# Optimization experiments

Measured on AMD Instinct MI355X. Metric: run time of the kernel, lower is better.

## Reference

```python
import jax, jax.numpy as jnp
import numpy as np

N, IN_DIM, OUT_DIM = 100000, 256, 256
EPS = 1e-6

def setup_inputs() -> dict:
    key = jax.random.key(0)
    ks = jax.random.split(key, 7)
    s = 1.0 / np.sqrt(IN_DIM)
    x = jax.random.normal(ks[0], (N, IN_DIM), dtype=jnp.float32)
    Wq = jax.random.uniform(ks[1], (IN_DIM, OUT_DIM), jnp.float32, -s, s)
    bq = jax.random.uniform(ks[2], (OUT_DIM,), jnp.float32, -s, s)
    Wk = jax.random.uniform(ks[3], (IN_DIM, OUT_DIM), jnp.float32, -s, s)
    bk = jax.random.uniform(ks[4], (OUT_DIM,), jnp.float32, -s, s)
    Wv = jax.random.uniform(ks[5], (IN_DIM, OUT_DIM), jnp.float32, -s, s)
    bv = jax.random.uniform(ks[6], (OUT_DIM,), jnp.float32, -s, s)
    return {"x": x, "Wq": Wq, "bq": bq, "Wk": Wk, "bk": bk, "Wv": Wv, "bv": bv}

def reference(x, Wq, bq, Wk, bk, Wv, bv):
    Q = jax.nn.relu(x @ Wq + bq)          # [N, d]
    K = jax.nn.relu(x @ Wk + bk)          # [N, d]
    V = x @ Wv + bv                       # [N, d]
    KV = jnp.einsum('nd,ne->de', K, V)    # [d, d]
    out = Q @ KV                          # [N, d]
    normalizer = Q @ K.sum(axis=0)[:, None].reshape(-1) [..., None] if False else (Q @ K.sum(axis=0)[:, None]) + EPS  # [N, 1]
    return out / normalizer
```

## Files before the change

### kernel.cpp

```cpp
#include <hip/hip_runtime.h>

typedef unsigned short u16;
typedef float f32x4 __attribute__((ext_vector_type(4)));
typedef short s16x8 __attribute__((ext_vector_type(8)));
typedef unsigned short u16x4 __attribute__((ext_vector_type(4)));

#define EPS 1e-6f

static __device__ __forceinline__ u16 f2bf(float f) {
  unsigned u = __float_as_uint(f);
  u += 0x7fffu + ((u >> 16) & 1u);
  return (u16)(u >> 16);
}
static __device__ __forceinline__ float bf2f(u16 h) {
  return __uint_as_float(((unsigned)h) << 16);
}

__global__ void wtrans_kernel(const float* __restrict__ Wq, const float* __restrict__ Wk,
                              const float* __restrict__ Wv,
                              u16* __restrict__ WqT, u16* __restrict__ WkT, u16* __restrict__ WvT) {
  int b = blockIdx.x;
  int mat = b >> 4, cg = b & 15;
  const float* W = mat == 0 ? Wq : (mat == 1 ? Wk : Wv);
  u16* WT = mat == 0 ? WqT : (mat == 1 ? WkT : WvT);
  int t = threadIdx.x;
  int c = cg * 16 + (t & 15);
  int k0 = (t >> 4) * 16;
  for (int i = 0; i < 16; ++i) {
    int k = k0 + i;
    WT[c * 256 + k] = f2bf(W[k * 256 + c]);
  }
}

__global__ __launch_bounds__(256, 2)
void qkv_kernel(const float* __restrict__ x,
                const u16* __restrict__ WqT, const u16* __restrict__ WkT, const u16* __restrict__ WvT,
                const float* __restrict__ bq, const float* __restrict__ bk, const float* __restrict__ bv,
                u16* __restrict__ Qb, u16* __restrict__ Kt, u16* __restrict__ Vt,
                int N, int NPAD) {
  __shared__ u16 xs[128][264];
  __shared__ u16 wst[128][40];
  const int tid = threadIdx.x;
  const int n0 = blockIdx.x * 128;

  for (int i = 0; i < 32; ++i) {
    int l = tid + i * 256;
    int row = l >> 6;
    int c4 = (l & 63) << 2;
    int n = n0 + row;
    float4 v = make_float4(0.f, 0.f, 0.f, 0.f);
    if (n < N) v = *(const float4*)(x + (size_t)n * 256 + c4);
    xs[row][c4 + 0] = f2bf(v.x);
    xs[row][c4 + 1] = f2bf(v.y);
    xs[row][c4 + 2] = f2bf(v.z);
    xs[row][c4 + 3] = f2bf(v.w);
  }

  const int wave = tid >> 6, lane = tid & 63;
  const int quad = lane >> 4, l16 = lane & 15;
  const int wr = (wave >> 1) * 64;
  const int wc = (wave & 1) * 64;

  for (int ph = 0; ph < 6; ++ph) {
    const int mat = ph >> 1;
    const int colBase = (ph & 1) * 128;
    const u16* WT = mat == 0 ? WqT : (mat == 1 ? WkT : WvT);
    const float* bias = mat == 0 ? bq : (mat == 1 ? bk : bv);
    f32x4 acc[4][4] = {};
    for (int kc = 0; kc < 256; kc += 32) {
      __syncthreads();
      for (int i = 0; i < 2; ++i) {
        int l = tid + i * 256;
        int col = l >> 2;
        int seg = (l & 3) << 3;
        *(s16x8*)&wst[col][seg] = *(const s16x8*)&WT[(size_t)(colBase + col) * 256 + kc + seg];
      }
      __syncthreads();
      s16x8 a[4], b[4];
      for (int f = 0; f < 4; ++f) a[f] = *(const s16x8*)&xs[wr + f * 16 + l16][kc + quad * 8];
      for (int f = 0; f < 4; ++f) b[f] = *(const s16x8*)&wst[wc + f * 16 + l16][quad * 8];
      for (int fr = 0; fr < 4; ++fr)
        for (int fc = 0; fc < 4; ++fc)
          acc[fr][fc] = __builtin_amdgcn_mfma_f32_16x16x32_bf16(a[fr], b[fc], acc[fr][fc], 0, 0, 0);
    }
    for (int fc = 0; fc < 4; ++fc) {
      int colg = colBase + wc + fc * 16 + l16;
      float bb = bias[colg];
      for (int fr = 0; fr < 4; ++fr) {
        int nl = wr + fr * 16 + quad * 4;
        int n = n0 + nl;
        if (mat == 0) {
          for (int j = 0; j < 4; ++j) {
            float v = acc[fr][fc][j] + bb;
            v = fmaxf(v, 0.f);
            Qb[(size_t)(n + j) * 256 + colg] = (n + j < N) ? f2bf(v) : (u16)0;
          }
        } else {
          u16x4 pk;
          for (int j = 0; j < 4; ++j) {
            float v = acc[fr][fc][j] + bb;
            if (mat == 1) v = fmaxf(v, 0.f);
            pk[j] = (n + j < N) ? f2bf(v) : (u16)0;
          }
          u16* T = (mat == 1) ? Kt : Vt;
          *(u16x4*)&T[(size_t)colg * NPAD + n] = pk;
        }
      }
    }
  }
}

__global__ void ksum_kernel(const u16* __restrict__ Kt, float* __restrict__ ksum, int NPAD) {
  int d = blockIdx.x;
  int t = threadIdx.x;
  const u16* row = Kt + (size_t)d * NPAD;
  float s = 0.f;
  int nu = NPAD >> 3;
  for (int j = t; j < nu; j += 256) {
    s16x8 v = *(const s16x8*)(row + j * 8);
    for (int e = 0; e < 8; ++e) s += bf2f((u16)v[e]);
  }
  for (int off = 32; off > 0; off >>= 1) s += __shfl_down(s, off);
  __shared__ float red[4];
  if ((t & 63) == 0) red[t >> 6] = s;
  __syncthreads();
  if (t == 0) ksum[d] = red[0] + red[1] + red[2] + red[3];
}

__global__ __launch_bounds__(256, 2)
void kv_kernel(const u16* __restrict__ Kt, const u16* __restrict__ Vt,
               float* __restrict__ P, int NPAD) {
  __shared__ u16 As[128][40];
  __shared__ u16 Bs[128][40];
  const int tid = threadIdx.x;
  const int s = blockIdx.x & 63;
  const int tile = blockIdx.x >> 6;
  const int ti = (tile >> 1) * 128;
  const int tj = (tile & 1) * 128;
  const int wave = tid >> 6, lane = tid & 63;
  const int quad = lane >> 4, l16 = lane & 15;
  const int we = (wave >> 1) * 64;
  const int wd = (wave & 1) * 64;
  f32x4 acc[4][4] = {};
  const int NCH = NPAD >> 5;
  for (int c = s; c < NCH; c += 64) {
    int nb = c << 5;
    __syncthreads();
    for (int i = 0; i < 2; ++i) {
      int l = tid + i * 256;
      int row = l >> 2;
      int seg = (l & 3) << 3;
      *(s16x8*)&As[row][seg] = *(const s16x8*)&Vt[(size_t)(ti + row) * NPAD + nb + seg];
      *(s16x8*)&Bs[row][seg] = *(const s16x8*)&Kt[(size_t)(tj + row) * NPAD + nb + seg];
    }
    __syncthreads();
    s16x8 a[4], b[4];
    for (int f = 0; f < 4; ++f) a[f] = *(const s16x8*)&As[we + f * 16 + l16][quad * 8];
    for (int f = 0; f < 4; ++f) b[f] = *(const s16x8*)&Bs[wd + f * 16 + l16][quad * 8];
    for (int fr = 0; fr < 4; ++fr)
      for (int fc = 0; fc < 4; ++fc)
        acc[fr][fc] = __builtin_amdgcn_mfma_f32_16x16x32_bf16(a[fr], b[fc], acc[fr][fc], 0, 0, 0);
  }
  float* Pp = P + (size_t)s * 65536;
  for (int fr = 0; fr < 4; ++fr)
    for (int fc = 0; fc < 4; ++fc) {
      int d = tj + wd + fc * 16 + l16;
      int e0 = ti + we + fr * 16 + quad * 4;
      *(f32x4*)&Pp[(size_t)d * 256 + e0] = acc[fr][fc];
    }
}

__global__ void kvred_kernel(const float* __restrict__ P, u16* __restrict__ KVtb) {
  int d = blockIdx.x;
  int e = threadIdx.x;
  float s = 0.f;
  for (int sp = 0; sp < 64; ++sp) s += P[(size_t)sp * 65536 + d * 256 + e];
  KVtb[e * 256 + d] = f2bf(s);
}

__global__ __launch_bounds__(256, 2)
void out_kernel(const u16* __restrict__ Qb, const u16* __restrict__ KVtb,
                const float* __restrict__ ksum, float* __restrict__ out,
                int N, int NPAD) {
  __shared__ u16 Qs[128][264];
  __shared__ u16 KVs[128][40];
  __shared__ float nrm[128];
  __shared__ float ks[256];
  const int tid = threadIdx.x;
  const int r0 = blockIdx.x * 128;

  for (int i = 0; i < 16; ++i) {
    int l = tid + i * 256;
    int row = l >> 5;
    int seg = (l & 31) << 3;
    *(s16x8*)&Qs[row][seg] = *(const s16x8*)&Qb[(size_t)(r0 + row) * 256 + seg];
  }
  ks[tid] = ksum[tid];
  __syncthreads();
  if (tid < 128) {
    float sacc = 0.f;
    for (int d = 0; d < 256; ++d) sacc += bf2f(Qs[tid][d]) * ks[d];
    nrm[tid] = sacc + EPS;
  }

  const int wave = tid >> 6, lane = tid & 63;
  const int quad = lane >> 4, l16 = lane & 15;
  const int we = (wave >> 1) * 64;
  const int wrw = (wave & 1) * 64;
  for (int eh = 0; eh < 2; ++eh) {
    f32x4 acc[4][4] = {};
    for (int kc = 0; kc < 256; kc += 32) {
      __syncthreads();
      for (int i = 0; i < 2; ++i) {
        int l = tid + i * 256;
        int row = l >> 2;
        int seg = (l & 3) << 3;
        *(s16x8*)&KVs[row][seg] = *(const s16x8*)&KVtb[(size_t)(eh * 128 + row) * 256 + kc + seg];
      }
      __syncthreads();
      s16x8 a[4], b[4];
      for (int f = 0; f < 4; ++f) a[f] = *(const s16x8*)&KVs[we + f * 16 + l16][quad * 8];
      for (int f = 0; f < 4; ++f) b[f] = *(const s16x8*)&Qs[wrw + f * 16 + l16][kc + quad * 8];
      for (int fr = 0; fr < 4; ++fr)
        for (int fc = 0; fc < 4; ++fc)
          acc[fr][fc] = __builtin_amdgcn_mfma_f32_16x16x32_bf16(a[fr], b[fc], acc[fr][fc], 0, 0, 0);
    }
    for (int fc = 0; fc < 4; ++fc) {
      int rl = wrw + fc * 16 + l16;
      int rg = r0 + rl;
      float inv = 1.0f / nrm[rl];
      if (rg < N) {
        for (int fr = 0; fr < 4; ++fr) {
          int eg = eh * 128 + we + fr * 16 + quad * 4;
          f32x4 o;
          o[0] = acc[fr][fc][0] * inv;
          o[1] = acc[fr][fc][1] * inv;
          o[2] = acc[fr][fc][2] * inv;
          o[3] = acc[fr][fc][3] * inv;
          *(f32x4*)&out[(size_t)rg * 256 + eg] = o;
        }
      }
    }
  }
}

extern "C" void kernel_launch(void* const* d_in, const int* in_sizes, int n_in,
                              void* d_out, int out_size, void* d_ws, size_t ws_size,
                              hipStream_t stream) {
  const float* x  = (const float*)d_in[0];
  const float* Wq = (const float*)d_in[1];
  const float* bq = (const float*)d_in[2];
  const float* Wk = (const float*)d_in[3];
  const float* bk = (const float*)d_in[4];
  const float* Wv = (const float*)d_in[5];
  const float* bv = (const float*)d_in[6];
  float* out = (float*)d_out;

  int N = in_sizes[0] / 256;
  int NPAD = ((N + 127) / 128) * 128;
  int nblk = NPAD / 128;

  char* p = (char*)d_ws;
  size_t szT = (size_t)256 * NPAD * sizeof(u16);
  u16* Kt = (u16*)p; p += szT;
  u16* Vt = (u16*)p; p += szT;
  u16* Qb = (u16*)p; p += szT;
  float* P = (float*)p; p += (size_t)64 * 65536 * sizeof(float);
  u16* KVtb = (u16*)p; p += (size_t)65536 * sizeof(u16);
  float* ksum = (float*)p; p += 256 * sizeof(float);
  u16* WqT = (u16*)p; p += (size_t)65536 * sizeof(u16);
  u16* WkT = (u16*)p; p += (size_t)65536 * sizeof(u16);
  u16* WvT = (u16*)p; p += (size_t)65536 * sizeof(u16);

  wtrans_kernel<<<48, 256, 0, stream>>>(Wq, Wk, Wv, WqT, WkT, WvT);
  qkv_kernel<<<nblk, 256, 0, stream>>>(x, WqT, WkT, WvT, bq, bk, bv, Qb, Kt, Vt, N, NPAD);
  ksum_kernel<<<256, 256, 0, stream>>>(Kt, ksum, NPAD);
  kv_kernel<<<256, 256, 0, stream>>>(Kt, Vt, P, NPAD);
  kvred_kernel<<<256, 256, 0, stream>>>(P, KVtb);
  out_kernel<<<nblk, 256, 0, stream>>>(Qb, KVtb, ksum, out, N, NPAD);
}
```

Before: 398.2 us.

## Fuse K column-sum into QKV GEMM and load weights directly into registers

Removes the separate ksum kernel by accumulating column sums of relu(K) in the QKV epilogue through shared-memory and global atomics, with a memset to zero the buffer first. The QKV and output GEMMs now load weight and KV fragments straight from global memory into registers instead of staging them through shared memory, which removes per-chunk barriers. The KV kernel prefetches the next chunk into registers while computing the current one, and the normalizer dot product is split across all 256 threads. Side effects: the K sum is taken from fp32 values rather than bf16-rounded ones, atomic order makes it nondeterministic, and register pressure rises.

```diff
diff --git a/kernel.cpp b/kernel.cpp
--- a/kernel.cpp
+++ b/kernel.cpp
@@ -37,11 +37,13 @@
                 const u16* __restrict__ WqT, const u16* __restrict__ WkT, const u16* __restrict__ WvT,
                 const float* __restrict__ bq, const float* __restrict__ bk, const float* __restrict__ bv,
                 u16* __restrict__ Qb, u16* __restrict__ Kt, u16* __restrict__ Vt,
-                int N, int NPAD) {
+                float* __restrict__ ksum, int N, int NPAD) {
   __shared__ u16 xs[128][264];
-  __shared__ u16 wst[128][40];
+  __shared__ float ksl[256];
   const int tid = threadIdx.x;
   const int n0 = blockIdx.x * 128;
+
+  ksl[tid] = 0.f;
 
   for (int i = 0; i < 32; ++i) {
     int l = tid + i * 256;
@@ -55,6 +57,7 @@
     xs[row][c4 + 2] = f2bf(v.z);
     xs[row][c4 + 3] = f2bf(v.w);
   }
+  __syncthreads();
 
   const int wave = tid >> 6, lane = tid & 63;
   const int quad = lane >> 4, l16 = lane & 15;
@@ -67,22 +70,25 @@
     const u16* WT = mat == 0 ? WqT : (mat == 1 ? WkT : WvT);
     const float* bias = mat == 0 ? bq : (mat == 1 ? bk : bv);
     f32x4 acc[4][4] = {};
-    for (int kc = 0; kc < 256; kc += 32) {
-      __syncthreads();
-      for (int i = 0; i < 2; ++i) {
-        int l = tid + i * 256;
-        int col = l >> 2;
-        int seg = (l & 3) << 3;
-        *(s16x8*)&wst[col][seg] = *(const s16x8*)&WT[(size_t)(colBase + col) * 256 + kc + seg];
-      }
-      __syncthreads();
-      s16x8 a[4], b[4];
-      for (int f = 0; f < 4; ++f) a[f] = *(const s16x8*)&xs[wr + f * 16 + l16][kc + quad * 8];
-      for (int f = 0; f < 4; ++f) b[f] = *(const s16x8*)&wst[wc + f * 16 + l16][quad * 8];
-      for (int fr = 0; fr < 4; ++fr)
-        for (int fc = 0; fc < 4; ++fc)
-          acc[fr][fc] = __builtin_amdgcn_mfma_f32_16x16x32_bf16(a[fr], b[fc], acc[fr][fc], 0, 0, 0);
-    }
+
+    for (int half = 0; half < 2; ++half) {
+      s16x8 breg[4][4];
+      for (int fc = 0; fc < 4; ++fc) {
+        const u16* colp = WT + (size_t)(colBase + wc + fc * 16 + l16) * 256 + quad * 8;
+        for (int kc2 = 0; kc2 < 4; ++kc2)
+          breg[kc2][fc] = *(const s16x8*)(colp + (half * 4 + kc2) * 32);
+      }
+      for (int kc2 = 0; kc2 < 4; ++kc2) {
+        int kc = (half * 4 + kc2) * 32;
+        s16x8 a[4];
+        for (int f = 0; f < 4; ++f) a[f] = *(const s16x8*)&xs[wr + f * 16 + l16][kc + quad * 8];
+        for (int fr = 0; fr < 4; ++fr)
+          for (int fc = 0; fc < 4; ++fc)
+            acc[fr][fc] = __builtin_amdgcn_mfma_f32_16x16x32_bf16(a[fr], breg[kc2][fc], acc[fr][fc], 0, 0, 0);
+      }
+    }
+
+    float ksacc[4] = {0.f, 0.f, 0.f, 0.f};
     for (int fc = 0; fc < 4; ++fc) {
       int colg = colBase + wc + fc * 16 + l16;
       float bb = bias[colg];
@@ -100,38 +106,33 @@
           for (int j = 0; j < 4; ++j) {
             float v = acc[fr][fc][j] + bb;
             if (mat == 1) v = fmaxf(v, 0.f);
-            pk[j] = (n + j < N) ? f2bf(v) : (u16)0;
+            bool ok = (n + j < N);
+            pk[j] = ok ? f2bf(v) : (u16)0;
+            if (mat == 1) ksacc[fc] += ok ? v : 0.f;
           }
           u16* T = (mat == 1) ? Kt : Vt;
           *(u16x4*)&T[(size_t)colg * NPAD + n] = pk;
         }
       }
     }
-  }
-}
-
-__global__ void ksum_kernel(const u16* __restrict__ Kt, float* __restrict__ ksum, int NPAD) {
-  int d = blockIdx.x;
-  int t = threadIdx.x;
-  const u16* row = Kt + (size_t)d * NPAD;
-  float s = 0.f;
-  int nu = NPAD >> 3;
-  for (int j = t; j < nu; j += 256) {
-    s16x8 v = *(const s16x8*)(row + j * 8);
-    for (int e = 0; e < 8; ++e) s += bf2f((u16)v[e]);
-  }
-  for (int off = 32; off > 0; off >>= 1) s += __shfl_down(s, off);
-  __shared__ float red[4];
-  if ((t & 63) == 0) red[t >> 6] = s;
-  __syncthreads();
-  if (t == 0) ksum[d] = red[0] + red[1] + red[2] + red[3];
+    if (mat == 1) {
+      for (int fc = 0; fc < 4; ++fc) {
+        float v = ksacc[fc];
+        v += __shfl_xor(v, 16);
+        v += __shfl_xor(v, 32);
+        if (quad == 0) atomicAdd(&ksl[colBase + wc + fc * 16 + l16], v);
+      }
+    }
+  }
+  __syncthreads();
+  atomicAdd(&ksum[tid], ksl[tid]);
 }
 
 __global__ __launch_bounds__(256, 2)
 void kv_kernel(const u16* __restrict__ Kt, const u16* __restrict__ Vt,
                float* __restrict__ P, int NPAD) {
-  __shared__ u16 As[128][40];
-  __shared__ u16 Bs[128][40];
+  __shared__ u16 As[128 * 32];
+  __shared__ u16 Bs[128 * 32];
   const int tid = threadIdx.x;
   const int s = blockIdx.x & 63;
   const int tile = blockIdx.x >> 6;
@@ -143,20 +144,37 @@
   const int wd = (wave & 1) * 64;
   f32x4 acc[4][4] = {};
   const int NCH = NPAD >> 5;
-  for (int c = s; c < NCH; c += 64) {
+
+  int row0 = (tid * 2) >> 2, seg0 = ((tid * 2) & 3) * 8;
+  int row1 = (tid * 2 + 1) >> 2, seg1 = ((tid * 2 + 1) & 3) * 8;
+
+  s16x8 ra0, ra1, rb0, rb1;
+  int c = s;
+  if (c < NCH) {
     int nb = c << 5;
+    ra0 = *(const s16x8*)&Vt[(size_t)(ti + row0) * NPAD + nb + seg0];
+    ra1 = *(const s16x8*)&Vt[(size_t)(ti + row1) * NPAD + nb + seg1];
+    rb0 = *(const s16x8*)&Kt[(size_t)(tj + row0) * NPAD + nb + seg0];
+    rb1 = *(const s16x8*)&Kt[(size_t)(tj + row1) * NPAD + nb + seg1];
+  }
+  for (; c < NCH; c += 64) {
     __syncthreads();
-    for (int i = 0; i < 2; ++i) {
-      int l = tid + i * 256;
-      int row = l >> 2;
-      int seg = (l & 3) << 3;
-      *(s16x8*)&As[row][seg] = *(const s16x8*)&Vt[(size_t)(ti + row) * NPAD + nb + seg];
-      *(s16x8*)&Bs[row][seg] = *(const s16x8*)&Kt[(size_t)(tj + row) * NPAD + nb + seg];
-    }
+    *(s16x8*)&As[row0 * 32 + seg0] = ra0;
+    *(s16x8*)&As[row1 * 32 + seg1] = ra1;
+    *(s16x8*)&Bs[row0 * 32 + seg0] = rb0;
+    *(s16x8*)&Bs[row1 * 32 + seg1] = rb1;
     __syncthreads();
+    int cn = c + 64;
+    if (cn < NCH) {
+      int nb = cn << 5;
+      ra0 = *(const s16x8*)&Vt[(size_t)(ti + row0) * NPAD + nb + seg0];
+      ra1 = *(const s16x8*)&Vt[(size_t)(ti + row1) * NPAD + nb + seg1];
+      rb0 = *(const s16x8*)&Kt[(size_t)(tj + row0) * NPAD + nb + seg0];
+      rb1 = *(const s16x8*)&Kt[(size_t)(tj + row1) * NPAD + nb + seg1];
+    }
     s16x8 a[4], b[4];
-    for (int f = 0; f < 4; ++f) a[f] = *(const s16x8*)&As[we + f * 16 + l16][quad * 8];
-    for (int f = 0; f < 4; ++f) b[f] = *(const s16x8*)&Bs[wd + f * 16 + l16][quad * 8];
+    for (int f = 0; f < 4; ++f) a[f] = *(const s16x8*)&As[(we + f * 16 + l16) * 32 + quad * 8];
+    for (int f = 0; f < 4; ++f) b[f] = *(const s16x8*)&Bs[(wd + f * 16 + l16) * 32 + quad * 8];
     for (int fr = 0; fr < 4; ++fr)
       for (int fc = 0; fc < 4; ++fc)
         acc[fr][fc] = __builtin_amdgcn_mfma_f32_16x16x32_bf16(a[fr], b[fc], acc[fr][fc], 0, 0, 0);
@@ -183,9 +201,9 @@
                 const float* __restrict__ ksum, float* __restrict__ out,
                 int N, int NPAD) {
   __shared__ u16 Qs[128][264];
-  __shared__ u16 KVs[128][40];
   __shared__ float nrm[128];
   __shared__ float ks[256];
+  __shared__ float nrmp[256];
   const int tid = threadIdx.x;
   const int r0 = blockIdx.x * 128;
 
@@ -197,11 +215,19 @@
   }
   ks[tid] = ksum[tid];
   __syncthreads();
-  if (tid < 128) {
-    float sacc = 0.f;
-    for (int d = 0; d < 256; ++d) sacc += bf2f(Qs[tid][d]) * ks[d];
-    nrm[tid] = sacc + EPS;
-  }
+
+  {
+    int r = tid & 127, h = tid >> 7;
+    float sa = 0.f;
+    for (int d = h * 128; d < h * 128 + 128; d += 8) {
+      s16x8 q = *(const s16x8*)&Qs[r][d];
+      for (int j = 0; j < 8; ++j) sa += bf2f((u16)q[j]) * ks[d + j];
+    }
+    nrmp[tid] = sa;
+  }
+  __syncthreads();
+  if (tid < 128) nrm[tid] = nrmp[tid] + nrmp[tid + 128] + EPS;
+  __syncthreads();
 
   const int wave = tid >> 6, lane = tid & 63;
   const int quad = lane >> 4, l16 = lane & 15;
@@ -209,21 +235,21 @@
   const int wrw = (wave & 1) * 64;
   for (int eh = 0; eh < 2; ++eh) {
     f32x4 acc[4][4] = {};
-    for (int kc = 0; kc < 256; kc += 32) {
-      __syncthreads();
-      for (int i = 0; i < 2; ++i) {
-        int l = tid + i * 256;
-        int row = l >> 2;
-        int seg = (l & 3) << 3;
-        *(s16x8*)&KVs[row][seg] = *(const s16x8*)&KVtb[(size_t)(eh * 128 + row) * 256 + kc + seg];
-      }
-      __syncthreads();
-      s16x8 a[4], b[4];
-      for (int f = 0; f < 4; ++f) a[f] = *(const s16x8*)&KVs[we + f * 16 + l16][quad * 8];
-      for (int f = 0; f < 4; ++f) b[f] = *(const s16x8*)&Qs[wrw + f * 16 + l16][kc + quad * 8];
-      for (int fr = 0; fr < 4; ++fr)
-        for (int fc = 0; fc < 4; ++fc)
-          acc[fr][fc] = __builtin_amdgcn_mfma_f32_16x16x32_bf16(a[fr], b[fc], acc[fr][fc], 0, 0, 0);
+    for (int half = 0; half < 2; ++half) {
+      s16x8 areg[4][4];
+      for (int fr = 0; fr < 4; ++fr) {
+        const u16* rowp = KVtb + (size_t)(eh * 128 + we + fr * 16 + l16) * 256 + quad * 8;
+        for (int kc2 = 0; kc2 < 4; ++kc2)
+          areg[kc2][fr] = *(const s16x8*)(rowp + (half * 4 + kc2) * 32);
+      }
+      for (int kc2 = 0; kc2 < 4; ++kc2) {
+        int kc = (half * 4 + kc2) * 32;
+        s16x8 b[4];
+        for (int f = 0; f < 4; ++f) b[f] = *(const s16x8*)&Qs[wrw + f * 16 + l16][kc + quad * 8];
+        for (int fr = 0; fr < 4; ++fr)
+          for (int fc = 0; fc < 4; ++fc)
+            acc[fr][fc] = __builtin_amdgcn_mfma_f32_16x16x32_bf16(areg[kc2][fr], b[fc], acc[fr][fc], 0, 0, 0);
+      }
     }
     for (int fc = 0; fc < 4; ++fc) {
       int rl = wrw + fc * 16 + l16;
@@ -272,9 +298,9 @@
   u16* WkT = (u16*)p; p += (size_t)65536 * sizeof(u16);
   u16* WvT = (u16*)p; p += (size_t)65536 * sizeof(u16);
 
+  hipMemsetAsync(ksum, 0, 256 * sizeof(float), stream);
   wtrans_kernel<<<48, 256, 0, stream>>>(Wq, Wk, Wv, WqT, WkT, WvT);
-  qkv_kernel<<<nblk, 256, 0, stream>>>(x, WqT, WkT, WvT, bq, bk, bv, Qb, Kt, Vt, N, NPAD);
-  ksum_kernel<<<256, 256, 0, stream>>>(Kt, ksum, NPAD);
+  qkv_kernel<<<nblk, 256, 0, stream>>>(x, WqT, WkT, WvT, bq, bk, bv, Qb, Kt, Vt, ksum, N, NPAD);
   kv_kernel<<<256, 256, 0, stream>>>(Kt, Vt, P, NPAD);
   kvred_kernel<<<256, 256, 0, stream>>>(P, KVtb);
   out_kernel<<<nblk, 256, 0, stream>>>(Qb, KVtb, ksum, out, N, NPAD);
```

After: 470.6 us. 1.18x slower.
